# Performance work log

Hardware: AMD Instinct MI355X
Metric: run time of the kernel (lower is better)

## Reference

```python
import jax, jax.numpy as jnp
import numpy as np

N_NODES = 50000
N_EDGES = 600000
D_IN = 128
D_HID = 128
D_OUT = 47
BN_EPS = 1e-5


def setup_inputs() -> dict:
    key = jax.random.key(0)
    ks = jax.random.split(key, 16)
    x = jax.random.normal(ks[0], (N_NODES, D_IN), dtype=jnp.float32)
    edge_index = jax.random.randint(ks[1], (2, N_EDGES), 0, N_NODES, dtype=jnp.int64)
    s = 0.05
    return {
        'x': x,
        'edge_index': edge_index,
        # SAGEConv layer 1: lin_l (neighbor agg, with bias), lin_r (root, no bias)
        'W1l': jax.random.normal(ks[2], (D_IN, D_HID), jnp.float32) * s,
        'b1': jnp.zeros((D_HID,), jnp.float32),
        'W1r': jax.random.normal(ks[3], (D_IN, D_HID), jnp.float32) * s,
        # layer 2
        'W2l': jax.random.normal(ks[4], (D_HID, D_HID), jnp.float32) * s,
        'b2': jnp.zeros((D_HID,), jnp.float32),
        'W2r': jax.random.normal(ks[5], (D_HID, D_HID), jnp.float32) * s,
        # layer 3
        'W3l': jax.random.normal(ks[6], (D_HID, D_OUT), jnp.float32) * s,
        'b3': jnp.zeros((D_OUT,), jnp.float32),
        'W3r': jax.random.normal(ks[7], (D_HID, D_OUT), jnp.float32) * s,
        # BatchNorm params (eval mode: running stats)
        'g1': jnp.ones((D_HID,), jnp.float32),
        'be1': jnp.zeros((D_HID,), jnp.float32),
        'm1': jax.random.normal(ks[8], (D_HID,), jnp.float32) * 0.1,
        'v1': jnp.ones((D_HID,), jnp.float32) + jax.random.uniform(ks[9], (D_HID,)) * 0.1,
        'g2': jnp.ones((D_HID,), jnp.float32),
        'be2': jnp.zeros((D_HID,), jnp.float32),
        'm2': jax.random.normal(ks[10], (D_HID,), jnp.float32) * 0.1,
        'v2': jnp.ones((D_HID,), jnp.float32) + jax.random.uniform(ks[11], (D_HID,)) * 0.1,
    }


def _sage_conv(x, src, dst, Wl, b, Wr):
    # mean aggregation of source features at destination nodes
    n = x.shape[0]
    msg = x[src]  # [E, d] gather
    agg = jax.ops.segment_sum(msg, dst, num_segments=n)
    cnt = jax.ops.segment_sum(jnp.ones((src.shape[0],), x.dtype), dst, num_segments=n)
    agg = agg / jnp.maximum(cnt, 1.0)[:, None]  # zero in-degree -> 0
    return agg @ Wl + b + x @ Wr


def _bn_eval(x, g, be, m, v):
    return (x - m) * (g * jax.lax.rsqrt(v + BN_EPS)) + be


def reference(x, edge_index, W1l, b1, W1r, W2l, b2, W2r, W3l, b3, W3r,
              g1, be1, m1, v1, g2, be2, m2, v2):
    src, dst = edge_index[0], edge_index[1]
    h = _sage_conv(x, src, dst, W1l, b1, W1r)
    h = jax.nn.relu(_bn_eval(h, g1, be1, m1, v1))  # dropout is identity in eval
    h = _sage_conv(h, src, dst, W2l, b2, W2r)
    h = jax.nn.relu(_bn_eval(h, g2, be2, m2, v2))
    return _sage_conv(h, src, dst, W3l, b3, W3r)
```

## Files before the change

### kernel.cpp

```cpp
#include <hip/hip_runtime.h>

#define NN 50000
#define NE 600000
#define D 128
#define DOUT3 47
#define ZW 64
#define BN_EPS 1e-5f
#define NPB 256
#define SB 196

typedef __attribute__((ext_vector_type(8))) short short8;
typedef __attribute__((ext_vector_type(4))) float f32x4;

__device__ inline unsigned short f2b(float f) {
  union { float f; unsigned u; } c; c.f = f;
  unsigned u = c.u;
  unsigned r = (u + 0x7FFFu + ((u >> 16) & 1u)) >> 16;
  return (unsigned short)r;
}
__device__ inline float b2f(unsigned short h) {
  union { unsigned u; float f; } c; c.u = ((unsigned)h) << 16;
  return c.f;
}

__global__ void zero_int(int* __restrict__ p, int n) {
  int i = blockIdx.x * blockDim.x + threadIdx.x;
  if (i < n) p[i] = 0;
}

__global__ __launch_bounds__(256) void prep_hist(
    const float4* __restrict__ x4, unsigned short* __restrict__ xb,
    const float* __restrict__ W1l, const float* __restrict__ W1r, unsigned short* __restrict__ Bt1,
    const float* __restrict__ W2l, const float* __restrict__ W2r, unsigned short* __restrict__ Bt2,
    const float* __restrict__ W3l, const float* __restrict__ W3r, unsigned short* __restrict__ Bt3,
    const int* __restrict__ dst, int* __restrict__ deg) {
  int b = blockIdx.x;
  int t = threadIdx.x;
  if (b < 1024) {
    long n4 = (long)NN * D / 4;
    for (long i = (long)b * 256 + t; i < n4; i += 1024L * 256) {
      float4 v = x4[i];
      uint2 p;
      p.x = (unsigned)f2b(v.x) | ((unsigned)f2b(v.y) << 16);
      p.y = (unsigned)f2b(v.z) | ((unsigned)f2b(v.w) << 16);
      *(uint2*)(xb + i * 4) = p;
    }
  } else if (b < 1280) {
    const float* Wl = (b < 1152) ? W1l : W2l;
    const float* Wr = (b < 1152) ? W1r : W2r;
    unsigned short* Bt = (b < 1152) ? Bt1 : Bt2;
    int idx = ((b < 1152) ? (b - 1024) : (b - 1152)) * 256 + t;
    int j = idx >> 8, k = idx & 255;
    float v = (k < 128) ? Wl[k * D + j] : Wr[(k - 128) * D + j];
    Bt[idx] = f2b(v);
  } else if (b < 1336) {
    int idx = (b - 1280) * 256 + t;
    if (idx < 112 * 128) {
      int j = idx >> 7, k = idx & 127;
      float v = 0.f;
      if (j < DOUT3) v = W3l[k * DOUT3 + j];
      else if (j >= 64 && j < 64 + DOUT3) v = W3r[k * DOUT3 + (j - 64)];
      Bt3[idx] = f2b(v);
    }
  } else {
    int e = (b - 1336) * 256 + t;
    if (e < NE) {
      int d = dst[e];
      d = max(0, min(NN - 1, d));
      atomicAdd(&deg[d], 1);
    }
  }
}

__global__ __launch_bounds__(NPB) void scan_local(const int* __restrict__ deg,
                                                  int* __restrict__ row_start,
                                                  int* __restrict__ partials) {
  __shared__ int s[NPB];
  int t = threadIdx.x;
  int i = blockIdx.x * NPB + t;
  int v = (i < NN) ? deg[i] : 0;
  s[t] = v;
  __syncthreads();
  for (int off = 1; off < NPB; off <<= 1) {
    int u = (t >= off) ? s[t - off] : 0;
    __syncthreads();
    s[t] += u;
    __syncthreads();
  }
  if (i < NN) row_start[i] = s[t] - v;
  if (t == NPB - 1) partials[blockIdx.x] = s[NPB - 1];
}

__global__ __launch_bounds__(NPB) void scan_add(int* __restrict__ row_start,
                                                const int* __restrict__ partials,
                                                int* __restrict__ cursor) {
  __shared__ int s[NPB];
  int t = threadIdx.x;
  int v = (t < SB) ? partials[t] : 0;
  s[t] = v;
  __syncthreads();
  for (int off = 1; off < NPB; off <<= 1) {
    int u = (t >= off) ? s[t - off] : 0;
    __syncthreads();
    s[t] += u;
    __syncthreads();
  }
  int base = s[blockIdx.x] - partials[blockIdx.x];
  int i = blockIdx.x * NPB + t;
  if (i < NN) {
    int r = row_start[i] + base;
    row_start[i] = r;
    cursor[i] = r;
  }
  if (i == 0) row_start[NN] = NE;
}

__global__ void build_kernel(const int* __restrict__ src, const int* __restrict__ dst,
                             int* __restrict__ cursor, int* __restrict__ srcs, int E) {
  int e = blockIdx.x * blockDim.x + threadIdx.x;
  if (e < E) {
    int d = dst[e];
    d = max(0, min(NN - 1, d));
    int s = src[e];
    s = max(0, min(NN - 1, s));
    int pos = atomicAdd(&cursor[d], 1);
    srcs[pos] = s;
  }
}

template <bool TR>
__global__ __launch_bounds__(256) void fused_layer(
    const unsigned short* __restrict__ feat,
    const int* __restrict__ row_start, const int* __restrict__ srcs,
    const unsigned short* __restrict__ Bt, const float* __restrict__ bias,
    const float* __restrict__ g, const float* __restrict__ be,
    const float* __restrict__ m, const float* __restrict__ v,
    unsigned short* __restrict__ outb,
    const unsigned short* __restrict__ Bt3,
    const float* __restrict__ b3,
    unsigned short* __restrict__ Z,
    float* __restrict__ outP) {
  __shared__ __align__(16) unsigned short s_a[16][136];
  int tid = threadIdx.x;
  int row0 = blockIdx.x * 16;
  int grp = tid >> 4, s = tid & 15;
  const unsigned short* fp = feat + s * 8;

  {
    int node = row0 + grp;
    int start = row_start[node], end = row_start[node + 1];
    int last = end - 1;
    float a[8];
#pragma unroll
    for (int i = 0; i < 8; i++) a[i] = 0.f;
    for (int e = start; e < end; e += 8) {
      int i0 = srcs[e];
      int i1 = srcs[min(e + 1, last)];
      int i2 = srcs[min(e + 2, last)];
      int i3 = srcs[min(e + 3, last)];
      int i4 = srcs[min(e + 4, last)];
      int i5 = srcs[min(e + 5, last)];
      int i6 = srcs[min(e + 6, last)];
      int i7 = srcs[min(e + 7, last)];
      float w1 = (e + 1 < end) ? 1.f : 0.f;
      float w2 = (e + 2 < end) ? 1.f : 0.f;
      float w3 = (e + 3 < end) ? 1.f : 0.f;
      float w4 = (e + 4 < end) ? 1.f : 0.f;
      float w5 = (e + 5 < end) ? 1.f : 0.f;
      float w6 = (e + 6 < end) ? 1.f : 0.f;
      float w7 = (e + 7 < end) ? 1.f : 0.f;
      short8 v0 = *(const short8*)(fp + (long)i0 * D);
      short8 v1 = *(const short8*)(fp + (long)i1 * D);
      short8 v2 = *(const short8*)(fp + (long)i2 * D);
      short8 v3 = *(const short8*)(fp + (long)i3 * D);
      short8 v4 = *(const short8*)(fp + (long)i4 * D);
      short8 v5 = *(const short8*)(fp + (long)i5 * D);
      short8 v6 = *(const short8*)(fp + (long)i6 * D);
      short8 v7 = *(const short8*)(fp + (long)i7 * D);
#pragma unroll
      for (int i = 0; i < 8; i++) {
        float t0 = b2f((unsigned short)v0[i]) + w1 * b2f((unsigned short)v1[i]);
        float t1 = w2 * b2f((unsigned short)v2[i]) + w3 * b2f((unsigned short)v3[i]);
        float t2 = w4 * b2f((unsigned short)v4[i]) + w5 * b2f((unsigned short)v5[i]);
        float t3 = w6 * b2f((unsigned short)v6[i]) + w7 * b2f((unsigned short)v7[i]);
        a[i] += (t0 + t1) + (t2 + t3);
      }
    }
    float iv = 1.0f / fmaxf((float)(end - start), 1.0f);
    uint4 p;
    p.x = (unsigned)f2b(a[0] * iv) | ((unsigned)f2b(a[1] * iv) << 16);
    p.y = (unsigned)f2b(a[2] * iv) | ((unsigned)f2b(a[3] * iv) << 16);
    p.z = (unsigned)f2b(a[4] * iv) | ((unsigned)f2b(a[5] * iv) << 16);
    p.w = (unsigned)f2b(a[6] * iv) | ((unsigned)f2b(a[7] * iv) << 16);
    *(uint4*)&s_a[grp][s * 8] = p;
  }

  __syncthreads();

  int lane = tid & 63, wid = tid >> 6;
  int r15 = lane & 15, hi = lane >> 4;
  f32x4 acc[2];
  acc[0] = (f32x4)(0.f);
  acc[1] = (f32x4)(0.f);

  const unsigned short* As = &s_a[r15][hi * 8];
  const unsigned short* Ax = feat + (long)(row0 + r15) * D + hi * 8;
  const unsigned short* Bp = Bt + (long)(wid * 2) * 16 * 256 + (long)r15 * 256 + hi * 8;

#pragma unroll
  for (int kf = 0; kf < 8; kf++) {
    const int kk = kf * 32;
    short8 a = (kf < 4) ? *(const short8*)(As + kk)
                        : *(const short8*)(Ax + (kk - 128));
#pragma unroll
    for (int f = 0; f < 2; f++) {
      short8 b = *(const short8*)(Bp + (long)f * 16 * 256 + kk);
      acc[f] = __builtin_amdgcn_mfma_f32_16x16x32_bf16(a, b, acc[f], 0, 0, 0);
    }
  }

  unsigned short hv[8];
#pragma unroll
  for (int f = 0; f < 2; f++) {
    int col = wid * 32 + f * 16 + r15;
    float bj = bias[col];
    float sc = g[col] * rsqrtf(v[col] + BN_EPS);
    float sh = be[col] - m[col] * sc;
#pragma unroll
    for (int r = 0; r < 4; r++) {
      float val = fmaxf((acc[f][r] + bj) * sc + sh, 0.f);
      hv[f * 4 + r] = f2b(val);
    }
  }

  if (!TR) {
#pragma unroll
    for (int f = 0; f < 2; f++) {
      int col = wid * 32 + f * 16 + r15;
#pragma unroll
      for (int r = 0; r < 4; r++) {
        int row = row0 + hi * 4 + r;
        outb[(long)row * D + col] = hv[f * 4 + r];
      }
    }
  } else {
    __syncthreads();
#pragma unroll
    for (int f = 0; f < 2; f++) {
      int col = wid * 32 + f * 16 + r15;
#pragma unroll
      for (int r = 0; r < 4; r++) {
        s_a[hi * 4 + r][col] = hv[f * 4 + r];
      }
    }
    __syncthreads();

    f32x4 acc2[2];
    acc2[0] = (f32x4)(0.f);
    acc2[1] = (f32x4)(0.f);
    const unsigned short* Ah = &s_a[r15][hi * 8];
#pragma unroll
    for (int ff = 0; ff < 2; ff++) {
      int fidx = wid * 2 + ff;
      if (fidx >= 7) break;
      const unsigned short* Bp3 = Bt3 + (long)fidx * 16 * 128 + (long)r15 * 128 + hi * 8;
#pragma unroll
      for (int kf = 0; kf < 4; kf++) {
        const int kk = kf * 32;
        short8 a = *(const short8*)(Ah + kk);
        short8 b = *(const short8*)(Bp3 + kk);
        acc2[ff] = __builtin_amdgcn_mfma_f32_16x16x32_bf16(a, b, acc2[ff], 0, 0, 0);
      }
#pragma unroll
      for (int r = 0; r < 4; r++) {
        int row = row0 + hi * 4 + r;
        int col = fidx * 16 + r15;
        float val = acc2[ff][r];
        if (col < ZW) {
          Z[(long)row * ZW + col] = f2b(val);
        } else {
          int pc = col - 64;
          if (pc < DOUT3) outP[(long)row * DOUT3 + pc] = val + b3[pc];
        }
      }
    }
  }
}

__global__ __launch_bounds__(256) void gather_add47(const unsigned short* __restrict__ Z,
                                                    const int* __restrict__ row_start,
                                                    const int* __restrict__ srcs,
                                                    float* __restrict__ outP) {
  int t = blockIdx.x * blockDim.x + threadIdx.x;
  int node = t >> 4;
  int s = t & 15;
  if (node >= NN) return;
  int start = row_start[node], end = row_start[node + 1];
  int last = end - 1;
  float a[4];
#pragma unroll
  for (int i = 0; i < 4; i++) a[i] = 0.f;
  const unsigned short* zp = Z + s * 4;
  for (int e = start; e < end; e += 8) {
    int i0 = srcs[e];
    int i1 = srcs[min(e + 1, last)];
    int i2 = srcs[min(e + 2, last)];
    int i3 = srcs[min(e + 3, last)];
    int i4 = srcs[min(e + 4, last)];
    int i5 = srcs[min(e + 5, last)];
    int i6 = srcs[min(e + 6, last)];
    int i7 = srcs[min(e + 7, last)];
    float w1 = (e + 1 < end) ? 1.f : 0.f;
    float w2 = (e + 2 < end) ? 1.f : 0.f;
    float w3 = (e + 3 < end) ? 1.f : 0.f;
    float w4 = (e + 4 < end) ? 1.f : 0.f;
    float w5 = (e + 5 < end) ? 1.f : 0.f;
    float w6 = (e + 6 < end) ? 1.f : 0.f;
    float w7 = (e + 7 < end) ? 1.f : 0.f;
    uint2 u0 = *(const uint2*)(zp + (long)i0 * ZW);
    uint2 u1 = *(const uint2*)(zp + (long)i1 * ZW);
    uint2 u2 = *(const uint2*)(zp + (long)i2 * ZW);
    uint2 u3 = *(const uint2*)(zp + (long)i3 * ZW);
    uint2 u4 = *(const uint2*)(zp + (long)i4 * ZW);
    uint2 u5 = *(const uint2*)(zp + (long)i5 * ZW);
    uint2 u6 = *(const uint2*)(zp + (long)i6 * ZW);
    uint2 u7 = *(const uint2*)(zp + (long)i7 * ZW);
    a[0] += (b2f((unsigned short)u0.x) + w1 * b2f((unsigned short)u1.x)) +
            (w2 * b2f((unsigned short)u2.x) + w3 * b2f((unsigned short)u3.x)) +
            (w4 * b2f((unsigned short)u4.x) + w5 * b2f((unsigned short)u5.x)) +
            (w6 * b2f((unsigned short)u6.x) + w7 * b2f((unsigned short)u7.x));
    a[1] += (b2f((unsigned short)(u0.x >> 16)) + w1 * b2f((unsigned short)(u1.x >> 16))) +
            (w2 * b2f((unsigned short)(u2.x >> 16)) + w3 * b2f((unsigned short)(u3.x >> 16))) +
            (w4 * b2f((unsigned short)(u4.x >> 16)) + w5 * b2f((unsigned short)(u5.x >> 16))) +
            (w6 * b2f((unsigned short)(u6.x >> 16)) + w7 * b2f((unsigned short)(u7.x >> 16)));
    a[2] += (b2f((unsigned short)u0.y) + w1 * b2f((unsigned short)u1.y)) +
            (w2 * b2f((unsigned short)u2.y) + w3 * b2f((unsigned short)u3.y)) +
            (w4 * b2f((unsigned short)u4.y) + w5 * b2f((unsigned short)u5.y)) +
            (w6 * b2f((unsigned short)u6.y) + w7 * b2f((unsigned short)u7.y));
    a[3] += (b2f((unsigned short)(u0.y >> 16)) + w1 * b2f((unsigned short)(u1.y >> 16))) +
            (w2 * b2f((unsigned short)(u2.y >> 16)) + w3 * b2f((unsigned short)(u3.y >> 16))) +
            (w4 * b2f((unsigned short)(u4.y >> 16)) + w5 * b2f((unsigned short)(u5.y >> 16))) +
            (w6 * b2f((unsigned short)(u6.y >> 16)) + w7 * b2f((unsigned short)(u7.y >> 16)));
  }
  float iv = 1.0f / fmaxf((float)(end - start), 1.0f);
#pragma unroll
  for (int i = 0; i < 4; i++) {
    int c = s * 4 + i;
    if (c < DOUT3) {
      long o = (long)node * DOUT3 + c;
      outP[o] = outP[o] + a[i] * iv;
    }
  }
}

extern "C" void kernel_launch(void* const* d_in, const int* in_sizes, int n_in,
                              void* d_out, int out_size, void* d_ws, size_t ws_size,
                              hipStream_t stream) {
  const float* x = (const float*)d_in[0];
  const int* ei = (const int*)d_in[1];
  const int* src = ei;
  const int* dst = ei + NE;
  const float* W1l = (const float*)d_in[2];
  const float* b1  = (const float*)d_in[3];
  const float* W1r = (const float*)d_in[4];
  const float* W2l = (const float*)d_in[5];
  const float* b2  = (const float*)d_in[6];
  const float* W2r = (const float*)d_in[7];
  const float* W3l = (const float*)d_in[8];
  const float* b3  = (const float*)d_in[9];
  const float* W3r = (const float*)d_in[10];
  const float* g1  = (const float*)d_in[11];
  const float* be1 = (const float*)d_in[12];
  const float* m1  = (const float*)d_in[13];
  const float* v1  = (const float*)d_in[14];
  const float* g2  = (const float*)d_in[15];
  const float* be2 = (const float*)d_in[16];
  const float* m2  = (const float*)d_in[17];
  const float* v2  = (const float*)d_in[18];

  float* out = (float*)d_out;

  int* deg       = (int*)d_ws;
  int* row_start = deg + NN;
  int* cursor    = row_start + NN + 4;
  int* partials  = cursor + NN;
  int* srcs      = partials + 256;
  unsigned short* xb   = (unsigned short*)(srcs + NE);
  unsigned short* h1b  = xb + (long)NN * D;
  unsigned short* Zb   = h1b + (long)NN * D;
  unsigned short* Bt1  = Zb + (long)NN * ZW;
  unsigned short* Bt2  = Bt1 + 128 * 256;
  unsigned short* Bt3  = Bt2 + 128 * 256;

  zero_int<<<SB, 256, 0, stream>>>(deg, NN);
  prep_hist<<<3680, 256, 0, stream>>>(
      (const float4*)x, xb, W1l, W1r, Bt1, W2l, W2r, Bt2, W3l, W3r, Bt3, dst, deg);

  scan_local<<<SB, NPB, 0, stream>>>(deg, row_start, partials);
  scan_add<<<SB, NPB, 0, stream>>>(row_start, partials, cursor);
  build_kernel<<<(NE + 255) / 256, 256, 0, stream>>>(src, dst, cursor, srcs, NE);

  int tiles = NN / 16;

  fused_layer<false><<<tiles, 256, 0, stream>>>(
      xb, row_start, srcs, Bt1, b1, g1, be1, m1, v1, h1b,
      nullptr, nullptr, nullptr, nullptr);

  fused_layer<true><<<tiles, 256, 0, stream>>>(
      h1b, row_start, srcs, Bt2, b2, g2, be2, m2, v2, nullptr,
      Bt3, b3, Zb, out);

  gather_add47<<<(NN * 16 + 255) / 256, 256, 0, stream>>>(Zb, row_start, srcs, out);
}
```

Measured before the change: 216.2 us.

## Stage edge indices in LDS, software-pipeline gathers, overlap root GEMM with aggregation

Each 16-node tile first copies its contiguous CSR source-index range into shared memory, so the per-edge index loads in the fused layer and the final gather come from LDS rather than global memory. The neighbor gather loop is double-buffered so the next 8 feature rows are loaded while the current 8 are accumulated. The root (x @ Wr) half of the MFMA GEMM now runs before the barrier, overlapping it with other waves' aggregation. The cost is an extra barrier, more registers for the prefetch buffers (which may lower occupancy), and a fallback branch to global memory for tiles whose edge count exceeds the LDS capacity.

```diff
diff --git a/kernel.cpp b/kernel.cpp
--- a/kernel.cpp
+++ b/kernel.cpp
@@ -8,6 +8,7 @@
 #define BN_EPS 1e-5f
 #define NPB 256
 #define SB 196
+#define IDXCAP 512
 
 typedef __attribute__((ext_vector_type(8))) short short8;
 typedef __attribute__((ext_vector_type(4))) float f32x4;
@@ -141,51 +142,67 @@
     unsigned short* __restrict__ Z,
     float* __restrict__ outP) {
   __shared__ __align__(16) unsigned short s_a[16][136];
+  __shared__ int s_idx[IDXCAP];
   int tid = threadIdx.x;
   int row0 = blockIdx.x * 16;
   int grp = tid >> 4, s = tid & 15;
+  int lane = tid & 63, wid = tid >> 6;
+  int r15 = lane & 15, hi = lane >> 4;
   const unsigned short* fp = feat + s * 8;
+
+  int tstart = row_start[row0];
+  int tcnt = min(row_start[row0 + 16] - tstart, IDXCAP);
+  for (int i = tid; i < tcnt; i += 256) s_idx[i] = srcs[tstart + i];
+  __syncthreads();
 
   {
     int node = row0 + grp;
     int start = row_start[node], end = row_start[node + 1];
     int last = end - 1;
+    auto gidx = [&](int ee) -> int {
+      int o = ee - tstart;
+      return (o < IDXCAP) ? s_idx[o] : srcs[ee];
+    };
     float a[8];
 #pragma unroll
     for (int i = 0; i < 8; i++) a[i] = 0.f;
-    for (int e = start; e < end; e += 8) {
-      int i0 = srcs[e];
-      int i1 = srcs[min(e + 1, last)];
-      int i2 = srcs[min(e + 2, last)];
-      int i3 = srcs[min(e + 3, last)];
-      int i4 = srcs[min(e + 4, last)];
-      int i5 = srcs[min(e + 5, last)];
-      int i6 = srcs[min(e + 6, last)];
-      int i7 = srcs[min(e + 7, last)];
-      float w1 = (e + 1 < end) ? 1.f : 0.f;
-      float w2 = (e + 2 < end) ? 1.f : 0.f;
-      float w3 = (e + 3 < end) ? 1.f : 0.f;
-      float w4 = (e + 4 < end) ? 1.f : 0.f;
-      float w5 = (e + 5 < end) ? 1.f : 0.f;
-      float w6 = (e + 6 < end) ? 1.f : 0.f;
-      float w7 = (e + 7 < end) ? 1.f : 0.f;
-      short8 v0 = *(const short8*)(fp + (long)i0 * D);
-      short8 v1 = *(const short8*)(fp + (long)i1 * D);
-      short8 v2 = *(const short8*)(fp + (long)i2 * D);
-      short8 v3 = *(const short8*)(fp + (long)i3 * D);
-      short8 v4 = *(const short8*)(fp + (long)i4 * D);
-      short8 v5 = *(const short8*)(fp + (long)i5 * D);
-      short8 v6 = *(const short8*)(fp + (long)i6 * D);
-      short8 v7 = *(const short8*)(fp + (long)i7 * D);
+
+    short8 vv[8];
+    int e0 = start;
+#pragma unroll
+    for (int k = 0; k < 8; k++)
+      vv[k] = *(const short8*)(fp + (long)gidx(min(e0 + k, last)) * D);
+
+    for (;;) {
+      int e1 = e0 + 8;
+      bool more = e1 < end;
+      short8 nv[8];
+      if (more) {
+#pragma unroll
+        for (int k = 0; k < 8; k++)
+          nv[k] = *(const short8*)(fp + (long)gidx(min(e1 + k, last)) * D);
+      }
+      float w1 = (e0 + 1 < end) ? 1.f : 0.f;
+      float w2 = (e0 + 2 < end) ? 1.f : 0.f;
+      float w3 = (e0 + 3 < end) ? 1.f : 0.f;
+      float w4 = (e0 + 4 < end) ? 1.f : 0.f;
+      float w5 = (e0 + 5 < end) ? 1.f : 0.f;
+      float w6 = (e0 + 6 < end) ? 1.f : 0.f;
+      float w7 = (e0 + 7 < end) ? 1.f : 0.f;
 #pragma unroll
       for (int i = 0; i < 8; i++) {
-        float t0 = b2f((unsigned short)v0[i]) + w1 * b2f((unsigned short)v1[i]);
-        float t1 = w2 * b2f((unsigned short)v2[i]) + w3 * b2f((unsigned short)v3[i]);
-        float t2 = w4 * b2f((unsigned short)v4[i]) + w5 * b2f((unsigned short)v5[i]);
-        float t3 = w6 * b2f((unsigned short)v6[i]) + w7 * b2f((unsigned short)v7[i]);
+        float t0 = b2f((unsigned short)vv[0][i]) + w1 * b2f((unsigned short)vv[1][i]);
+        float t1 = w2 * b2f((unsigned short)vv[2][i]) + w3 * b2f((unsigned short)vv[3][i]);
+        float t2 = w4 * b2f((unsigned short)vv[4][i]) + w5 * b2f((unsigned short)vv[5][i]);
+        float t3 = w6 * b2f((unsigned short)vv[6][i]) + w7 * b2f((unsigned short)vv[7][i]);
         a[i] += (t0 + t1) + (t2 + t3);
       }
-    }
+      if (!more) break;
+      e0 = e1;
+#pragma unroll
+      for (int k = 0; k < 8; k++) vv[k] = nv[k];
+    }
+
     float iv = 1.0f / fmaxf((float)(end - start), 1.0f);
     uint4 p;
     p.x = (unsigned)f2b(a[0] * iv) | ((unsigned)f2b(a[1] * iv) << 16);
@@ -195,27 +212,33 @@
     *(uint4*)&s_a[grp][s * 8] = p;
   }
 
-  __syncthreads();
-
-  int lane = tid & 63, wid = tid >> 6;
-  int r15 = lane & 15, hi = lane >> 4;
   f32x4 acc[2];
   acc[0] = (f32x4)(0.f);
   acc[1] = (f32x4)(0.f);
-
-  const unsigned short* As = &s_a[r15][hi * 8];
   const unsigned short* Ax = feat + (long)(row0 + r15) * D + hi * 8;
   const unsigned short* Bp = Bt + (long)(wid * 2) * 16 * 256 + (long)r15 * 256 + hi * 8;
-
-#pragma unroll
-  for (int kf = 0; kf < 8; kf++) {
+#pragma unroll
+  for (int kf = 4; kf < 8; kf++) {
     const int kk = kf * 32;
-    short8 a = (kf < 4) ? *(const short8*)(As + kk)
-                        : *(const short8*)(Ax + (kk - 128));
+    short8 aa = *(const short8*)(Ax + (kk - 128));
 #pragma unroll
     for (int f = 0; f < 2; f++) {
       short8 b = *(const short8*)(Bp + (long)f * 16 * 256 + kk);
-      acc[f] = __builtin_amdgcn_mfma_f32_16x16x32_bf16(a, b, acc[f], 0, 0, 0);
+      acc[f] = __builtin_amdgcn_mfma_f32_16x16x32_bf16(aa, b, acc[f], 0, 0, 0);
+    }
+  }
+
+  __syncthreads();
+
+  const unsigned short* As = &s_a[r15][hi * 8];
+#pragma unroll
+  for (int kf = 0; kf < 4; kf++) {
+    const int kk = kf * 32;
+    short8 aa = *(const short8*)(As + kk);
+#pragma unroll
+    for (int f = 0; f < 2; f++) {
+      short8 b = *(const short8*)(Bp + (long)f * 16 * 256 + kk);
+      acc[f] = __builtin_amdgcn_mfma_f32_16x16x32_bf16(aa, b, acc[f], 0, 0, 0);
     }
   }
 
@@ -267,9 +290,9 @@
 #pragma unroll
       for (int kf = 0; kf < 4; kf++) {
         const int kk = kf * 32;
-        short8 a = *(const short8*)(Ah + kk);
+        short8 aa = *(const short8*)(Ah + kk);
         short8 b = *(const short8*)(Bp3 + kk);
-        acc2[ff] = __builtin_amdgcn_mfma_f32_16x16x32_bf16(a, b, acc2[ff], 0, 0, 0);
+        acc2[ff] = __builtin_amdgcn_mfma_f32_16x16x32_bf16(aa, b, acc2[ff], 0, 0, 0);
       }
 #pragma unroll
       for (int r = 0; r < 4; r++) {
@@ -291,25 +314,35 @@
                                                     const int* __restrict__ row_start,
                                                     const int* __restrict__ srcs,
                                                     float* __restrict__ outP) {
-  int t = blockIdx.x * blockDim.x + threadIdx.x;
-  int node = t >> 4;
-  int s = t & 15;
-  if (node >= NN) return;
+  __shared__ int s_idx[IDXCAP];
+  int tid = threadIdx.x;
+  int row0 = blockIdx.x * 16;
+  int tstart = row_start[row0];
+  int tcnt = min(row_start[row0 + 16] - tstart, IDXCAP);
+  for (int i = tid; i < tcnt; i += 256) s_idx[i] = srcs[tstart + i];
+  __syncthreads();
+
+  int node = row0 + (tid >> 4);
+  int s = tid & 15;
   int start = row_start[node], end = row_start[node + 1];
   int last = end - 1;
+  auto gidx = [&](int ee) -> int {
+    int o = ee - tstart;
+    return (o < IDXCAP) ? s_idx[o] : srcs[ee];
+  };
   float a[4];
 #pragma unroll
   for (int i = 0; i < 4; i++) a[i] = 0.f;
   const unsigned short* zp = Z + s * 4;
   for (int e = start; e < end; e += 8) {
-    int i0 = srcs[e];
-    int i1 = srcs[min(e + 1, last)];
-    int i2 = srcs[min(e + 2, last)];
-    int i3 = srcs[min(e + 3, last)];
-    int i4 = srcs[min(e + 4, last)];
-    int i5 = srcs[min(e + 5, last)];
-    int i6 = srcs[min(e + 6, last)];
-    int i7 = srcs[min(e + 7, last)];
+    int i0 = gidx(e);
+    int i1 = gidx(min(e + 1, last));
+    int i2 = gidx(min(e + 2, last));
+    int i3 = gidx(min(e + 3, last));
+    int i4 = gidx(min(e + 4, last));
+    int i5 = gidx(min(e + 5, last));
+    int i6 = gidx(min(e + 6, last));
+    int i7 = gidx(min(e + 7, last));
     float w1 = (e + 1 < end) ? 1.f : 0.f;
     float w2 = (e + 2 < end) ? 1.f : 0.f;
     float w3 = (e + 3 < end) ? 1.f : 0.f;
@@ -410,5 +443,5 @@
       h1b, row_start, srcs, Bt2, b2, g2, be2, m2, v2, nullptr,
       Bt3, b3, Zb, out);
 
-  gather_add47<<<(NN * 16 + 255) / 256, 256, 0, stream>>>(Zb, row_start, srcs, out);
-}
+  gather_add47<<<tiles, 256, 0, stream>>>(Zb, row_start, srcs, out);
+}
```

Result: no change. 215.6 us (-0.3%).

## Split fused gather+GEMM into column-sliced gather kernel and separate GEMM kernel

Applied to the files above, without the earlier changes.

Splits the neighbor-mean aggregation out of the fused layer kernel into a standalone gather kernel. Each block handles one 32-column slice for 32 nodes, with 8 threads per node loading 8-byte chunks and using nontemporal loads of the edge indices. The aggregate is written to a bf16 buffer in global memory, which a separate GEMM kernel then reads. The aim is higher memory-level parallelism and better L2 locality per column slice. The cost is an extra round trip of an NN×128 bf16 buffer through memory, two more kernel launches, and re-reading srcs once per slice.

```diff
diff --git a/kernel.cpp b/kernel.cpp
--- a/kernel.cpp
+++ b/kernel.cpp
@@ -8,6 +8,7 @@
 #define BN_EPS 1e-5f
 #define NPB 256
 #define SB 196
+#define NSEG 1563
 
 typedef __attribute__((ext_vector_type(8))) short short8;
 typedef __attribute__((ext_vector_type(4))) float f32x4;
@@ -128,10 +129,51 @@
   }
 }
 
-template <bool TR>
-__global__ __launch_bounds__(256) void fused_layer(
+__global__ __launch_bounds__(256) void gather_slice(
     const unsigned short* __restrict__ feat,
     const int* __restrict__ row_start, const int* __restrict__ srcs,
+    unsigned short* __restrict__ agg) {
+  int cb = blockIdx.x & 3;
+  int node = (blockIdx.x >> 2) * 32 + (threadIdx.x >> 3);
+  int l = threadIdx.x & 7;
+  if (node >= NN) return;
+  int start = row_start[node], end = row_start[node + 1];
+  int last = end - 1;
+  const unsigned short* fp = feat + cb * 32 + l * 4;
+  float a0 = 0.f, a1 = 0.f, a2 = 0.f, a3 = 0.f;
+  for (int e = start; e < end; e += 8) {
+    int idx[8];
+    idx[0] = __builtin_nontemporal_load(srcs + e);
+#pragma unroll
+    for (int k = 1; k < 8; k++)
+      idx[k] = __builtin_nontemporal_load(srcs + min(e + k, last));
+    uint2 u[8];
+#pragma unroll
+    for (int k = 0; k < 8; k++)
+      u[k] = *(const uint2*)(fp + (long)idx[k] * D);
+    float w[8];
+    w[0] = 1.f;
+#pragma unroll
+    for (int k = 1; k < 8; k++) w[k] = (e + k < end) ? 1.f : 0.f;
+#pragma unroll
+    for (int k = 0; k < 8; k++) {
+      a0 += w[k] * b2f((unsigned short)u[k].x);
+      a1 += w[k] * b2f((unsigned short)(u[k].x >> 16));
+      a2 += w[k] * b2f((unsigned short)u[k].y);
+      a3 += w[k] * b2f((unsigned short)(u[k].y >> 16));
+    }
+  }
+  float iv = 1.0f / fmaxf((float)(end - start), 1.0f);
+  unsigned lo = (unsigned)f2b(a0 * iv) | ((unsigned)f2b(a1 * iv) << 16);
+  unsigned hiu = (unsigned)f2b(a2 * iv) | ((unsigned)f2b(a3 * iv) << 16);
+  unsigned long long o = (unsigned long long)lo | ((unsigned long long)hiu << 32);
+  __builtin_nontemporal_store(
+      o, (unsigned long long*)(agg + (long)node * D + cb * 32 + l * 4));
+}
+
+template <bool TR>
+__global__ __launch_bounds__(256) void gemm_tile(
+    const unsigned short* __restrict__ aggb, const unsigned short* __restrict__ feat,
     const unsigned short* __restrict__ Bt, const float* __restrict__ bias,
     const float* __restrict__ g, const float* __restrict__ be,
     const float* __restrict__ m, const float* __restrict__ v,
@@ -140,77 +182,24 @@
     const float* __restrict__ b3,
     unsigned short* __restrict__ Z,
     float* __restrict__ outP) {
-  __shared__ __align__(16) unsigned short s_a[16][136];
+  __shared__ __align__(16) unsigned short s_h[TR ? 16 : 1][136];
   int tid = threadIdx.x;
   int row0 = blockIdx.x * 16;
-  int grp = tid >> 4, s = tid & 15;
-  const unsigned short* fp = feat + s * 8;
-
-  {
-    int node = row0 + grp;
-    int start = row_start[node], end = row_start[node + 1];
-    int last = end - 1;
-    float a[8];
-#pragma unroll
-    for (int i = 0; i < 8; i++) a[i] = 0.f;
-    for (int e = start; e < end; e += 8) {
-      int i0 = srcs[e];
-      int i1 = srcs[min(e + 1, last)];
-      int i2 = srcs[min(e + 2, last)];
-      int i3 = srcs[min(e + 3, last)];
-      int i4 = srcs[min(e + 4, last)];
-      int i5 = srcs[min(e + 5, last)];
-      int i6 = srcs[min(e + 6, last)];
-      int i7 = srcs[min(e + 7, last)];
-      float w1 = (e + 1 < end) ? 1.f : 0.f;
-      float w2 = (e + 2 < end) ? 1.f : 0.f;
-      float w3 = (e + 3 < end) ? 1.f : 0.f;
-      float w4 = (e + 4 < end) ? 1.f : 0.f;
-      float w5 = (e + 5 < end) ? 1.f : 0.f;
-      float w6 = (e + 6 < end) ? 1.f : 0.f;
-      float w7 = (e + 7 < end) ? 1.f : 0.f;
-      short8 v0 = *(const short8*)(fp + (long)i0 * D);
-      short8 v1 = *(const short8*)(fp + (long)i1 * D);
-      short8 v2 = *(const short8*)(fp + (long)i2 * D);
-      short8 v3 = *(const short8*)(fp + (long)i3 * D);
-      short8 v4 = *(const short8*)(fp + (long)i4 * D);
-      short8 v5 = *(const short8*)(fp + (long)i5 * D);
-      short8 v6 = *(const short8*)(fp + (long)i6 * D);
-      short8 v7 = *(const short8*)(fp + (long)i7 * D);
-#pragma unroll
-      for (int i = 0; i < 8; i++) {
-        float t0 = b2f((unsigned short)v0[i]) + w1 * b2f((unsigned short)v1[i]);
-        float t1 = w2 * b2f((unsigned short)v2[i]) + w3 * b2f((unsigned short)v3[i]);
-        float t2 = w4 * b2f((unsigned short)v4[i]) + w5 * b2f((unsigned short)v5[i]);
-        float t3 = w6 * b2f((unsigned short)v6[i]) + w7 * b2f((unsigned short)v7[i]);
-        a[i] += (t0 + t1) + (t2 + t3);
-      }
-    }
-    float iv = 1.0f / fmaxf((float)(end - start), 1.0f);
-    uint4 p;
-    p.x = (unsigned)f2b(a[0] * iv) | ((unsigned)f2b(a[1] * iv) << 16);
-    p.y = (unsigned)f2b(a[2] * iv) | ((unsigned)f2b(a[3] * iv) << 16);
-    p.z = (unsigned)f2b(a[4] * iv) | ((unsigned)f2b(a[5] * iv) << 16);
-    p.w = (unsigned)f2b(a[6] * iv) | ((unsigned)f2b(a[7] * iv) << 16);
-    *(uint4*)&s_a[grp][s * 8] = p;
-  }
-
-  __syncthreads();
-
   int lane = tid & 63, wid = tid >> 6;
   int r15 = lane & 15, hi = lane >> 4;
+
   f32x4 acc[2];
   acc[0] = (f32x4)(0.f);
   acc[1] = (f32x4)(0.f);
 
-  const unsigned short* As = &s_a[r15][hi * 8];
+  const unsigned short* Aa = aggb + (long)(row0 + r15) * D + hi * 8;
   const unsigned short* Ax = feat + (long)(row0 + r15) * D + hi * 8;
   const unsigned short* Bp = Bt + (long)(wid * 2) * 16 * 256 + (long)r15 * 256 + hi * 8;
 
 #pragma unroll
   for (int kf = 0; kf < 8; kf++) {
     const int kk = kf * 32;
-    short8 a = (kf < 4) ? *(const short8*)(As + kk)
+    short8 a = (kf < 4) ? *(const short8*)(Aa + kk)
                         : *(const short8*)(Ax + (kk - 128));
 #pragma unroll
     for (int f = 0; f < 2; f++) {
@@ -244,13 +233,12 @@
       }
     }
   } else {
-    __syncthreads();
 #pragma unroll
     for (int f = 0; f < 2; f++) {
       int col = wid * 32 + f * 16 + r15;
 #pragma unroll
       for (int r = 0; r < 4; r++) {
-        s_a[hi * 4 + r][col] = hv[f * 4 + r];
+        s_h[hi * 4 + r][col] = hv[f * 4 + r];
       }
     }
     __syncthreads();
@@ -258,7 +246,7 @@
     f32x4 acc2[2];
     acc2[0] = (f32x4)(0.f);
     acc2[1] = (f32x4)(0.f);
-    const unsigned short* Ah = &s_a[r15][hi * 8];
+    const unsigned short* Ah = &s_h[r15][hi * 8];
 #pragma unroll
     for (int ff = 0; ff < 2; ff++) {
       int fidx = wid * 2 + ff;
@@ -287,68 +275,48 @@
   }
 }
 
-__global__ __launch_bounds__(256) void gather_add47(const unsigned short* __restrict__ Z,
-                                                    const int* __restrict__ row_start,
-                                                    const int* __restrict__ srcs,
-                                                    float* __restrict__ outP) {
-  int t = blockIdx.x * blockDim.x + threadIdx.x;
-  int node = t >> 4;
-  int s = t & 15;
+__global__ __launch_bounds__(256) void gather_z(
+    const unsigned short* __restrict__ Z,
+    const int* __restrict__ row_start, const int* __restrict__ srcs,
+    float* __restrict__ outP) {
+  int cb = blockIdx.x & 1;
+  int node = (blockIdx.x >> 1) * 32 + (threadIdx.x >> 3);
+  int l = threadIdx.x & 7;
   if (node >= NN) return;
   int start = row_start[node], end = row_start[node + 1];
   int last = end - 1;
-  float a[4];
-#pragma unroll
-  for (int i = 0; i < 4; i++) a[i] = 0.f;
-  const unsigned short* zp = Z + s * 4;
+  const unsigned short* zp = Z + cb * 32 + l * 4;
+  float a0 = 0.f, a1 = 0.f, a2 = 0.f, a3 = 0.f;
   for (int e = start; e < end; e += 8) {
-    int i0 = srcs[e];
-    int i1 = srcs[min(e + 1, last)];
-    int i2 = srcs[min(e + 2, last)];
-    int i3 = srcs[min(e + 3, last)];
-    int i4 = srcs[min(e + 4, last)];
-    int i5 = srcs[min(e + 5, last)];
-    int i6 = srcs[min(e + 6, last)];
-    int i7 = srcs[min(e + 7, last)];
-    float w1 = (e + 1 < end) ? 1.f : 0.f;
-    float w2 = (e + 2 < end) ? 1.f : 0.f;
-    float w3 = (e + 3 < end) ? 1.f : 0.f;
-    float w4 = (e + 4 < end) ? 1.f : 0.f;
-    float w5 = (e + 5 < end) ? 1.f : 0.f;
-    float w6 = (e + 6 < end) ? 1.f : 0.f;
-    float w7 = (e + 7 < end) ? 1.f : 0.f;
-    uint2 u0 = *(const uint2*)(zp + (long)i0 * ZW);
-    uint2 u1 = *(const uint2*)(zp + (long)i1 * ZW);
-    uint2 u2 = *(const uint2*)(zp + (long)i2 * ZW);
-    uint2 u3 = *(const uint2*)(zp + (long)i3 * ZW);
-    uint2 u4 = *(const uint2*)(zp + (long)i4 * ZW);
-    uint2 u5 = *(const uint2*)(zp + (long)i5 * ZW);
-    uint2 u6 = *(const uint2*)(zp + (long)i6 * ZW);
-    uint2 u7 = *(const uint2*)(zp + (long)i7 * ZW);
-    a[0] += (b2f((unsigned short)u0.x) + w1 * b2f((unsigned short)u1.x)) +
-            (w2 * b2f((unsigned short)u2.x) + w3 * b2f((unsigned short)u3.x)) +
-            (w4 * b2f((unsigned short)u4.x) + w5 * b2f((unsigned short)u5.x)) +
-            (w6 * b2f((unsigned short)u6.x) + w7 * b2f((unsigned short)u7.x));
-    a[1] += (b2f((unsigned short)(u0.x >> 16)) + w1 * b2f((unsigned short)(u1.x >> 16))) +
-            (w2 * b2f((unsigned short)(u2.x >> 16)) + w3 * b2f((unsigned short)(u3.x >> 16))) +
-            (w4 * b2f((unsigned short)(u4.x >> 16)) + w5 * b2f((unsigned short)(u5.x >> 16))) +
-            (w6 * b2f((unsigned short)(u6.x >> 16)) + w7 * b2f((unsigned short)(u7.x >> 16)));
-    a[2] += (b2f((unsigned short)u0.y) + w1 * b2f((unsigned short)u1.y)) +
-            (w2 * b2f((unsigned short)u2.y) + w3 * b2f((unsigned short)u3.y)) +
-            (w4 * b2f((unsigned short)u4.y) + w5 * b2f((unsigned short)u5.y)) +
-            (w6 * b2f((unsigned short)u6.y) + w7 * b2f((unsigned short)u7.y));
-    a[3] += (b2f((unsigned short)(u0.y >> 16)) + w1 * b2f((unsigned short)(u1.y >> 16))) +
-            (w2 * b2f((unsigned short)(u2.y >> 16)) + w3 * b2f((unsigned short)(u3.y >> 16))) +
-            (w4 * b2f((unsigned short)(u4.y >> 16)) + w5 * b2f((unsigned short)(u5.y >> 16))) +
-            (w6 * b2f((unsigned short)(u6.y >> 16)) + w7 * b2f((unsigned short)(u7.y >> 16)));
+    int idx[8];
+    idx[0] = __builtin_nontemporal_load(srcs + e);
+#pragma unroll
+    for (int k = 1; k < 8; k++)
+      idx[k] = __builtin_nontemporal_load(srcs + min(e + k, last));
+    uint2 u[8];
+#pragma unroll
+    for (int k = 0; k < 8; k++)
+      u[k] = *(const uint2*)(zp + (long)idx[k] * ZW);
+    float w[8];
+    w[0] = 1.f;
+#pragma unroll
+    for (int k = 1; k < 8; k++) w[k] = (e + k < end) ? 1.f : 0.f;
+#pragma unroll
+    for (int k = 0; k < 8; k++) {
+      a0 += w[k] * b2f((unsigned short)u[k].x);
+      a1 += w[k] * b2f((unsigned short)(u[k].x >> 16));
+      a2 += w[k] * b2f((unsigned short)u[k].y);
+      a3 += w[k] * b2f((unsigned short)(u[k].y >> 16));
+    }
   }
   float iv = 1.0f / fmaxf((float)(end - start), 1.0f);
+  float av[4] = {a0 * iv, a1 * iv, a2 * iv, a3 * iv};
 #pragma unroll
   for (int i = 0; i < 4; i++) {
-    int c = s * 4 + i;
+    int c = cb * 32 + l * 4 + i;
     if (c < DOUT3) {
       long o = (long)node * DOUT3 + c;
-      outP[o] = outP[o] + a[i] * iv;
+      outP[o] = outP[o] + av[i];
     }
   }
 }
@@ -386,7 +354,8 @@
   int* partials  = cursor + NN;
   int* srcs      = partials + 256;
   unsigned short* xb   = (unsigned short*)(srcs + NE);
-  unsigned short* h1b  = xb + (long)NN * D;
+  unsigned short* aggb = xb + (long)NN * D;
+  unsigned short* h1b  = aggb + (long)NN * D;
   unsigned short* Zb   = h1b + (long)NN * D;
   unsigned short* Bt1  = Zb + (long)NN * ZW;
   unsigned short* Bt2  = Bt1 + 128 * 256;
@@ -402,13 +371,15 @@
 
   int tiles = NN / 16;
 
-  fused_layer<false><<<tiles, 256, 0, stream>>>(
-      xb, row_start, srcs, Bt1, b1, g1, be1, m1, v1, h1b,
+  gather_slice<<<4 * NSEG, 256, 0, stream>>>(xb, row_start, srcs, aggb);
+  gemm_tile<false><<<tiles, 256, 0, stream>>>(
+      aggb, xb, Bt1, b1, g1, be1, m1, v1, h1b,
       nullptr, nullptr, nullptr, nullptr);
 
-  fused_layer<true><<<tiles, 256, 0, stream>>>(
-      h1b, row_start, srcs, Bt2, b2, g2, be2, m2, v2, nullptr,
+  gather_slice<<<4 * NSEG, 256, 0, stream>>>(h1b, row_start, srcs, aggb);
+  gemm_tile<true><<<tiles, 256, 0, stream>>>(
+      aggb, h1b, Bt2, b2, g2, be2, m2, v2, nullptr,
       Bt3, b3, Zb, out);
 
-  gather_add47<<<(NN * 16 + 255) / 256, 256, 0, stream>>>(Zb, row_start, srcs, out);
-}
+  gather_z<<<2 * NSEG, 256, 0, stream>>>(Zb, row_start, srcs, out);
+}
```

Result: slower. 328.7 us (+52.0%).
